# Optimization experiments

Hardware: AMD Instinct MI355X
Metric: run time of the kernel (lower is better)

The kernel has to match this reference:

```python
import jax, jax.numpy as jnp
import numpy as np

BETA = 0.25  # commitment loss weight


def setup_inputs() -> dict:
    key = jax.random.key(0)
    k1, k2 = jax.random.split(key)
    N, K, d = 131072, 1024, 64
    z_e = jax.random.normal(k1, (N, d), dtype=jnp.float32)
    scale = 1.0 / np.sqrt(d)
    codebook = jax.random.uniform(k2, (K, d), minval=-scale, maxval=scale, dtype=jnp.float32)
    return {"z_e": z_e, "codebook": codebook}


def reference(z_e, codebook):
    d = codebook.shape[-1]
    flat = z_e.reshape(-1, d)                                  # (N, d)
    z_sq = jnp.sum(flat ** 2, axis=-1, keepdims=True)          # (N, 1)
    c_sq = jnp.sum(codebook ** 2, axis=-1)[None, :]            # (1, K)
    zc = flat @ codebook.T                                     # (N, K)
    dists = z_sq - 2.0 * zc + c_sq
    idx_flat = jnp.argmin(dists, axis=-1)                      # (N,)
    e_flat = codebook[idx_flat]                                # (N, d)
    z_q_flat_st = flat + jax.lax.stop_gradient(e_flat - flat)  # straight-through
    codebook_loss = jnp.mean((e_flat - jax.lax.stop_gradient(flat)) ** 2)
    commitment_loss = jnp.mean((jax.lax.stop_gradient(e_flat) - flat) ** 2)
    vq_loss = codebook_loss + BETA * commitment_loss
    indices = idx_flat.reshape(z_e.shape[:-1])
    z_q_st = z_q_flat_st.reshape(z_e.shape)
    return (indices, z_q_st, vq_loss)
```

## Files before the change

kernel.cpp:

```cpp
#include <hip/hip_runtime.h>
#include <stdint.h>

#define DIM 64
#define KC 1024
#define HALF 512
#define ROWS_PER_BLOCK 512
#define TAU 5.0e-4f
typedef float f32x4 __attribute__((ext_vector_type(4)));
typedef short short8 __attribute__((ext_vector_type(8)));

__device__ __forceinline__ unsigned short bf16_rn(float f) {
  union { float f; uint32_t u; } v; v.f = f;
  uint32_t u = v.u;
  uint32_t r = u + 0x7fffu + ((u >> 16) & 1u);
  return (unsigned short)(r >> 16);
}
__device__ __forceinline__ float bf16_f32(unsigned short h) {
  union { uint32_t u; float f; } v; v.u = ((uint32_t)h) << 16;
  return v.f;
}
__device__ __forceinline__ void gll16(const void* g, void* l) {
  __builtin_amdgcn_global_load_lds(
      (const __attribute__((address_space(1))) void*)g,
      (__attribute__((address_space(3))) void*)l, 16, 0, 0);
}

__global__ void k1_prep(const float* __restrict__ cb,
                        unsigned short* __restrict__ cb_hi,
                        unsigned short* __restrict__ cb_lo,
                        float* __restrict__ csqh) {
  const int k = blockIdx.x, j = threadIdx.x;
  const float c = cb[k * DIM + j];
  const unsigned short hi = bf16_rn(c);
  const float hif = bf16_f32(hi);
  cb_hi[k * DIM + j] = hi;
  cb_lo[k * DIM + j] = bf16_rn(c - hif);
  float s = c * c;
  #pragma unroll
  for (int off = 32; off >= 1; off >>= 1) s += __shfl_xor(s, off);
  if (j == 0) csqh[k] = -0.5f * s;
}

__launch_bounds__(1024, 4)
__global__ void k2_argmin(const float* __restrict__ z,
                          const unsigned short* __restrict__ cb_hi,
                          const unsigned short* __restrict__ cb_lo,
                          const float* __restrict__ csqh,
                          const float* __restrict__ cb,
                          float* __restrict__ out_idx,
                          float* __restrict__ zq,
                          unsigned char* __restrict__ fl,
                          float* __restrict__ partials) {
  __shared__ unsigned short lds_cb[2 * HALF * DIM];
  __shared__ float lds_csq[KC];
  __shared__ float wpart[16];

  const int tid  = threadIdx.x;
  const int lane = tid & 63;
  const int wv   = tid >> 6;
  const int lg   = lane >> 4;
  const int lr   = lane & 15;
  const int row0 = blockIdx.x * ROWS_PER_BLOCK;

#define STAGE(h)                                                              \
  {                                                                           \
    _Pragma("unroll")                                                         \
    for (int p = 0; p < 8; ++p) {                                             \
      const int linear = p * 1024 + tid;                                      \
      const int ch = linear & 7;                                              \
      const int cl = (linear >> 3) & (HALF - 1);                              \
      const int split = linear >> 12;                                         \
      const unsigned short* src =                                             \
          (split ? cb_lo : cb_hi) + ((h) * HALF + cl) * DIM + ((ch ^ (cl & 7)) * 8); \
      gll16(src, (char*)lds_cb + linear * 16);                                \
    }                                                                         \
  }

  STAGE(0);
  if (tid < KC / 4) ((f32x4*)lds_csq)[tid] = ((const f32x4*)csqh)[tid];

  short8 zhi[2][2], zlo[2][2];
  float zsq[2];
  #pragma unroll
  for (int rt = 0; rt < 2; ++rt) {
    const int row = row0 + wv * 32 + rt * 16 + lr;
    float sq = 0.0f;
    #pragma unroll
    for (int ks = 0; ks < 2; ++ks) {
      const float* p = z + (size_t)row * DIM + ks * 32 + lg * 8;
      const f32x4 va = *(const f32x4*)p;
      const f32x4 vb = *(const f32x4*)(p + 4);
      sq = fmaf(va[0], va[0], sq); sq = fmaf(va[1], va[1], sq);
      sq = fmaf(va[2], va[2], sq); sq = fmaf(va[3], va[3], sq);
      sq = fmaf(vb[0], vb[0], sq); sq = fmaf(vb[1], vb[1], sq);
      sq = fmaf(vb[2], vb[2], sq); sq = fmaf(vb[3], vb[3], sq);
      union { uint32_t w[4]; short8 s8; } H, L;
      #pragma unroll
      for (int pr = 0; pr < 4; ++pr) {
        const float f0 = (pr < 2) ? va[2 * pr]     : vb[2 * pr - 4];
        const float f1 = (pr < 2) ? va[2 * pr + 1] : vb[2 * pr - 3];
        const uint32_t u0 = __float_as_uint(f0);
        const uint32_t u1 = __float_as_uint(f1);
        H.w[pr] = __builtin_amdgcn_perm(u1, u0, 0x07060302u);
        const float l0 = f0 - __uint_as_float(u0 & 0xffff0000u);
        const float l1 = f1 - __uint_as_float(u1 & 0xffff0000u);
        uint32_t lw;
        asm("v_cvt_pk_bf16_f32 %0, %1, %2" : "=v"(lw) : "v"(l0), "v"(l1));
        L.w[pr] = lw;
      }
      zhi[rt][ks] = H.s8;
      zlo[rt][ks] = L.s8;
    }
    zsq[rt] = sq;
  }

  float M1[2] = {-3.0e38f, -3.0e38f}, M2[2] = {-3.0e38f, -3.0e38f};
  int I1[2] = {0, 0};

  const int offh0 = lr * 128 + ((lg)     ^ (lr & 7)) * 16;
  const int offh1 = lr * 128 + ((4 + lg) ^ (lr & 7)) * 16;
  const int offl0 = offh0 + HALF * 128;
  const int offl1 = offh1 + HALF * 128;

  #pragma unroll
  for (int h = 0; h < 2; ++h) {
    __syncthreads();
    #pragma unroll 2
    for (int ct = 0; ct < HALF / 16; ++ct) {
      const int cbase = h * HALF + ct * 16 + lg * 4;
      const f32x4 init = *(const f32x4*)&lds_csq[cbase];
      const char* base = (const char*)lds_cb + ct * 2048;
      const short8 ch0 = *(const short8*)(base + offh0);
      const short8 ch1 = *(const short8*)(base + offh1);
      const short8 cl0 = *(const short8*)(base + offl0);
      const short8 cl1 = *(const short8*)(base + offl1);
      #pragma unroll
      for (int rt = 0; rt < 2; ++rt) {
        f32x4 acc = init;
        acc = __builtin_amdgcn_mfma_f32_16x16x32_bf16(ch0, zhi[rt][0], acc, 0, 0, 0);
        acc = __builtin_amdgcn_mfma_f32_16x16x32_bf16(ch1, zhi[rt][1], acc, 0, 0, 0);
        acc = __builtin_amdgcn_mfma_f32_16x16x32_bf16(ch0, zlo[rt][0], acc, 0, 0, 0);
        acc = __builtin_amdgcn_mfma_f32_16x16x32_bf16(ch1, zlo[rt][1], acc, 0, 0, 0);
        acc = __builtin_amdgcn_mfma_f32_16x16x32_bf16(cl0, zhi[rt][0], acc, 0, 0, 0);
        acc = __builtin_amdgcn_mfma_f32_16x16x32_bf16(cl1, zhi[rt][1], acc, 0, 0, 0);
        #pragma unroll
        for (int j = 0; j < 4; ++j) {
          const float s = acc[j];
          M2[rt] = __builtin_amdgcn_fmed3f(s, M1[rt], M2[rt]);
          const bool take = s > M1[rt];
          M1[rt] = fmaxf(s, M1[rt]);
          I1[rt] = take ? (cbase + j) : I1[rt];
        }
      }
    }
    __syncthreads();
    if (h == 0) STAGE(1);
  }
#undef STAGE

  float M1b[2], M2b[2], loss01 = 0.0f;
  int idxr[2];
  #pragma unroll
  for (int rt = 0; rt < 2; ++rt) {
    float m1 = M1[rt], m2 = M2[rt];
    int i1 = I1[rt];
    #pragma unroll
    for (int off = 16; off <= 32; off <<= 1) {
      const float o1 = __shfl_xor(m1, off);
      const float o2 = __shfl_xor(m2, off);
      const int   oi = __shfl_xor(i1, off);
      m2 = fmaxf(fmaxf(m2, o2), fminf(m1, o1));
      const bool take = (o1 > m1) || (o1 == m1 && oi < i1);
      if (take) { m1 = o1; i1 = oi; }
    }
    float zs = zsq[rt];
    zs += __shfl_xor(zs, 16);
    zs += __shfl_xor(zs, 32);
    M1b[rt] = m1; M2b[rt] = m2; idxr[rt] = i1;
    loss01 += zs - 2.0f * m1;
  }

  int* idxL = (int*)lds_csq;
  if (lane < 16) {
    #pragma unroll
    for (int rt = 0; rt < 2; ++rt) {
      const int r = wv * 32 + rt * 16 + lr;
      out_idx[row0 + r] = (float)idxr[rt];
      idxL[r] = idxr[rt];
      fl[row0 + r] = (M1b[rt] - M2b[rt] < TAU) ? 1 : 0;
    }
  }
  float lsum = loss01;
  #pragma unroll
  for (int off = 1; off <= 32; off <<= 1) lsum += __shfl_xor(lsum, off);
  if (lane == 0) wpart[wv] = lsum * 0.25f;
  __syncthreads();
  if (tid == 0) {
    float s = 0.0f;
    #pragma unroll
    for (int i = 0; i < 16; ++i) s += wpart[i];
    partials[blockIdx.x] = s;
  }
  {
    const int r2 = tid >> 1, halfq = tid & 1;
    const int idx = idxL[r2];
    const f32x4* src = (const f32x4*)(cb + (size_t)idx * DIM + halfq * 32);
    f32x4* dst = (f32x4*)(zq + (size_t)(row0 + r2) * DIM + halfq * 32);
    #pragma unroll
    for (int j = 0; j < 8; ++j) dst[j] = src[j];
  }
}

__global__ void k3_rescue(const float* __restrict__ z,
                          const float* __restrict__ cb,
                          const float* __restrict__ csqh,
                          const unsigned char* __restrict__ fl,
                          float* __restrict__ out_idx,
                          float* __restrict__ zq,
                          int nstripes) {
  const int lane = threadIdx.x & 63;
  const int w = blockIdx.x * 4 + (threadIdx.x >> 6);
  const int nw = gridDim.x * 4;
  for (int s = w; s < nstripes; s += nw) {
    const int base = s * 64;
    unsigned long long mask = __ballot(fl[base + lane] != 0);
    while (mask) {
      const int bit = __ffsll(mask) - 1;
      mask &= mask - 1;
      const int row = base + bit;
      const f32x4* zr4 = (const f32x4*)(z + (size_t)row * DIM);
      float m1 = -3.0e38f;
      int i1 = 0;
      for (int kk = 0; kk < 16; ++kk) {
        const int k = lane * 16 + kk;
        const f32x4* cp = (const f32x4*)(cb + (size_t)k * DIM);
        float acc = csqh[k];
        #pragma unroll
        for (int j4 = 0; j4 < DIM / 4; ++j4) {
          const f32x4 c4 = cp[j4];
          const f32x4 z4 = zr4[j4];
          acc = fmaf(z4[0], c4[0], acc);
          acc = fmaf(z4[1], c4[1], acc);
          acc = fmaf(z4[2], c4[2], acc);
          acc = fmaf(z4[3], c4[3], acc);
        }
        if (acc > m1) { m1 = acc; i1 = k; }
      }
      #pragma unroll
      for (int off = 32; off >= 1; off >>= 1) {
        const float o1 = __shfl_xor(m1, off);
        const int   oi = __shfl_xor(i1, off);
        if (o1 > m1 || (o1 == m1 && oi < i1)) { m1 = o1; i1 = oi; }
      }
      if (lane == 0) out_idx[row] = (float)i1;
      if (lane < 16)
        ((f32x4*)(zq + (size_t)row * DIM))[lane] =
            ((const f32x4*)(cb + (size_t)i1 * DIM))[lane];
    }
  }
}

__global__ void k5_reduce(const float* __restrict__ partials,
                          float* __restrict__ loss_slot,
                          float scale, int nb) {
  __shared__ float wsum[4];
  const int tid = threadIdx.x;
  float s = 0.0f;
  for (int i = tid; i < nb / 4; i += 256) {
    const f32x4 v = ((const f32x4*)partials)[i];
    s += (v[0] + v[1]) + (v[2] + v[3]);
  }
  #pragma unroll
  for (int off = 32; off >= 1; off >>= 1) s += __shfl_xor(s, off);
  if ((tid & 63) == 0) wsum[tid >> 6] = s;
  __syncthreads();
  if (tid == 0) *loss_slot = (wsum[0] + wsum[1] + wsum[2] + wsum[3]) * scale;
}

extern "C" void kernel_launch(void* const* d_in, const int* in_sizes, int n_in,
                              void* d_out, int out_size, void* d_ws, size_t ws_size,
                              hipStream_t stream) {
  const float* z  = (const float*)d_in[0];
  const float* cb = (const float*)d_in[1];
  const int N = in_sizes[0] / DIM;

  float* out       = (float*)d_out;
  float* out_idx   = out;
  float* zq        = out + N;
  float* loss_slot = out + N + (size_t)N * DIM;

  unsigned short* cb_hi = (unsigned short*)d_ws;
  unsigned short* cb_lo = cb_hi + KC * DIM;
  float* csqh = (float*)(cb_lo + KC * DIM);
  float* partials = csqh + KC;
  unsigned char* fl = (unsigned char*)(partials + 256);

  const int nb2 = N / ROWS_PER_BLOCK;
  const float scale = 1.25f / ((float)N * (float)DIM);

  k1_prep<<<KC, DIM, 0, stream>>>(cb, cb_hi, cb_lo, csqh);
  k2_argmin<<<nb2, 1024, 0, stream>>>(z, cb_hi, cb_lo, csqh, cb, out_idx, zq, fl, partials);
  k3_rescue<<<256, 256, 0, stream>>>(z, cb, csqh, fl, out_idx, zq, N / 64);
  k5_reduce<<<1, 256, 0, stream>>>(partials, loss_slot, scale, nb2);
}
```

Before: 201.9 us.

## Track best 4-column group in MFMA loop, refine with fp32 exact epilogue

The argmin inner loop now reduces each 4-wide accumulator to a single max and tracks only the winning column group, not a per-element index. An fp32 epilogue recomputes the exact scores for the 4 candidates in that group, picks the winner and sets a tighter rescue threshold. The block size drops to 512 threads and 256 rows, with the codebook staged in four quarters. The separate loss-reduce kernel is folded into the rescue kernel to save a launch. The epilogue adds some global loads and more barriers. The second-best score is now tracked per group, so near ties with an entry from the same group are only caught when those 4 candidates are recomputed.

```diff
diff --git a/kernel.cpp b/kernel.cpp
--- a/kernel.cpp
+++ b/kernel.cpp
@@ -3,9 +3,11 @@
 
 #define DIM 64
 #define KC 1024
-#define HALF 512
-#define ROWS_PER_BLOCK 512
-#define TAU 5.0e-4f
+#define QTR 256
+#define NPASS (KC / QTR)
+#define RPB 256
+#define TAU 5.0e-5f
+
 typedef float f32x4 __attribute__((ext_vector_type(4)));
 typedef short short8 __attribute__((ext_vector_type(8)));
 
@@ -32,16 +34,15 @@
   const int k = blockIdx.x, j = threadIdx.x;
   const float c = cb[k * DIM + j];
   const unsigned short hi = bf16_rn(c);
-  const float hif = bf16_f32(hi);
   cb_hi[k * DIM + j] = hi;
-  cb_lo[k * DIM + j] = bf16_rn(c - hif);
+  cb_lo[k * DIM + j] = bf16_rn(c - bf16_f32(hi));
   float s = c * c;
   #pragma unroll
   for (int off = 32; off >= 1; off >>= 1) s += __shfl_xor(s, off);
   if (j == 0) csqh[k] = -0.5f * s;
 }
 
-__launch_bounds__(1024, 4)
+__launch_bounds__(512, 4)
 __global__ void k2_argmin(const float* __restrict__ z,
                           const unsigned short* __restrict__ cb_hi,
                           const unsigned short* __restrict__ cb_lo,
@@ -51,27 +52,26 @@
                           float* __restrict__ zq,
                           unsigned char* __restrict__ fl,
                           float* __restrict__ partials) {
-  __shared__ unsigned short lds_cb[2 * HALF * DIM];
+  __shared__ unsigned short lds_cb[2 * QTR * DIM];
   __shared__ float lds_csq[KC];
-  __shared__ float wpart[16];
 
   const int tid  = threadIdx.x;
   const int lane = tid & 63;
   const int wv   = tid >> 6;
   const int lg   = lane >> 4;
   const int lr   = lane & 15;
-  const int row0 = blockIdx.x * ROWS_PER_BLOCK;
-
-#define STAGE(h)                                                              \
+  const int row0 = blockIdx.x * RPB;
+
+#define STAGE(pp)                                                             \
   {                                                                           \
     _Pragma("unroll")                                                         \
-    for (int p = 0; p < 8; ++p) {                                             \
-      const int linear = p * 1024 + tid;                                      \
+    for (int p2 = 0; p2 < 8; ++p2) {                                          \
+      const int linear = p2 * 512 + tid;                                      \
       const int ch = linear & 7;                                              \
-      const int cl = (linear >> 3) & (HALF - 1);                              \
-      const int split = linear >> 12;                                         \
+      const int cl = (linear >> 3) & (QTR - 1);                               \
+      const int split = linear >> 11;                                         \
       const unsigned short* src =                                             \
-          (split ? cb_lo : cb_hi) + ((h) * HALF + cl) * DIM + ((ch ^ (cl & 7)) * 8); \
+          (split ? cb_lo : cb_hi) + ((pp) * QTR + cl) * DIM + ((ch ^ (cl & 7)) * 8); \
       gll16(src, (char*)lds_cb + linear * 16);                                \
     }                                                                         \
   }
@@ -115,19 +115,18 @@
   }
 
   float M1[2] = {-3.0e38f, -3.0e38f}, M2[2] = {-3.0e38f, -3.0e38f};
-  int I1[2] = {0, 0};
+  int C1[2] = {0, 0};
 
   const int offh0 = lr * 128 + ((lg)     ^ (lr & 7)) * 16;
   const int offh1 = lr * 128 + ((4 + lg) ^ (lr & 7)) * 16;
-  const int offl0 = offh0 + HALF * 128;
-  const int offl1 = offh1 + HALF * 128;
-
-  #pragma unroll
-  for (int h = 0; h < 2; ++h) {
+  const int offl0 = offh0 + QTR * 128;
+  const int offl1 = offh1 + QTR * 128;
+
+  for (int p = 0; p < NPASS; ++p) {
     __syncthreads();
-    #pragma unroll 2
-    for (int ct = 0; ct < HALF / 16; ++ct) {
-      const int cbase = h * HALF + ct * 16 + lg * 4;
+    #pragma unroll 4
+    for (int ct = 0; ct < QTR / 16; ++ct) {
+      const int cbase = p * QTR + ct * 16 + lg * 4;
       const f32x4 init = *(const f32x4*)&lds_csq[cbase];
       const char* base = (const char*)lds_cb + ct * 2048;
       const short8 ch0 = *(const short8*)(base + offh0);
@@ -143,69 +142,101 @@
         acc = __builtin_amdgcn_mfma_f32_16x16x32_bf16(ch1, zlo[rt][1], acc, 0, 0, 0);
         acc = __builtin_amdgcn_mfma_f32_16x16x32_bf16(cl0, zhi[rt][0], acc, 0, 0, 0);
         acc = __builtin_amdgcn_mfma_f32_16x16x32_bf16(cl1, zhi[rt][1], acc, 0, 0, 0);
-        #pragma unroll
-        for (int j = 0; j < 4; ++j) {
-          const float s = acc[j];
-          M2[rt] = __builtin_amdgcn_fmed3f(s, M1[rt], M2[rt]);
-          const bool take = s > M1[rt];
-          M1[rt] = fmaxf(s, M1[rt]);
-          I1[rt] = take ? (cbase + j) : I1[rt];
-        }
+        const float qm = fmaxf(fmaxf(acc[0], acc[1]), fmaxf(acc[2], acc[3]));
+        M2[rt] = __builtin_amdgcn_fmed3f(qm, M1[rt], M2[rt]);
+        const bool take = qm > M1[rt];
+        M1[rt] = fmaxf(qm, M1[rt]);
+        C1[rt] = take ? cbase : C1[rt];
       }
     }
     __syncthreads();
-    if (h == 0) STAGE(1);
+    if (p < NPASS - 1) STAGE(p + 1);
   }
 #undef STAGE
 
-  float M1b[2], M2b[2], loss01 = 0.0f;
-  int idxr[2];
+  float m1f[2], m2f[2], zsf[2];
+  int cwf[2];
   #pragma unroll
   for (int rt = 0; rt < 2; ++rt) {
     float m1 = M1[rt], m2 = M2[rt];
-    int i1 = I1[rt];
+    int c1 = C1[rt];
     #pragma unroll
     for (int off = 16; off <= 32; off <<= 1) {
       const float o1 = __shfl_xor(m1, off);
       const float o2 = __shfl_xor(m2, off);
-      const int   oi = __shfl_xor(i1, off);
+      const int   oc = __shfl_xor(c1, off);
       m2 = fmaxf(fmaxf(m2, o2), fminf(m1, o1));
-      const bool take = (o1 > m1) || (o1 == m1 && oi < i1);
-      if (take) { m1 = o1; i1 = oi; }
+      const bool take = (o1 > m1) || (o1 == m1 && oc < c1);
+      if (take) { m1 = o1; c1 = oc; }
     }
     float zs = zsq[rt];
     zs += __shfl_xor(zs, 16);
     zs += __shfl_xor(zs, 32);
-    M1b[rt] = m1; M2b[rt] = m2; idxr[rt] = i1;
-    loss01 += zs - 2.0f * m1;
-  }
-
-  int* idxL = (int*)lds_csq;
-  if (lane < 16) {
+    m1f[rt] = m1; m2f[rt] = m2; cwf[rt] = c1; zsf[rt] = zs;
+  }
+
+  float* m2S   = (float*)lds_cb;
+  int*   cwS   = (int*)(m2S + 256);
+  float* zsS   = (float*)(cwS + 256);
+  float* lossS = zsS + 256;
+  int*   jS    = (int*)(lossS + 256);
+
+  if (lg == 0) {
     #pragma unroll
     for (int rt = 0; rt < 2; ++rt) {
       const int r = wv * 32 + rt * 16 + lr;
-      out_idx[row0 + r] = (float)idxr[rt];
-      idxL[r] = idxr[rt];
-      fl[row0 + r] = (M1b[rt] - M2b[rt] < TAU) ? 1 : 0;
-    }
-  }
-  float lsum = loss01;
-  #pragma unroll
-  for (int off = 1; off <= 32; off <<= 1) lsum += __shfl_xor(lsum, off);
-  if (lane == 0) wpart[wv] = lsum * 0.25f;
+      m2S[r] = m2f[rt];
+      cwS[r] = cwf[rt];
+      zsS[r] = zsf[rt];
+    }
+  }
   __syncthreads();
-  if (tid == 0) {
-    float s = 0.0f;
-    #pragma unroll
-    for (int i = 0; i < 16; ++i) s += wpart[i];
-    partials[blockIdx.x] = s;
-  }
+
   {
-    const int r2 = tid >> 1, halfq = tid & 1;
-    const int idx = idxL[r2];
-    const f32x4* src = (const f32x4*)(cb + (size_t)idx * DIM + halfq * 32);
-    f32x4* dst = (f32x4*)(zq + (size_t)(row0 + r2) * DIM + halfq * 32);
+    const int row = tid >> 1, pr = tid & 1;
+    const int cw = cwS[row];
+    const int c0 = cw + pr * 2, c1i = c0 + 1;
+    const f32x4* zr4 = (const f32x4*)(z + (size_t)(row0 + row) * DIM);
+    const f32x4* cb0 = (const f32x4*)(cb + (size_t)c0 * DIM);
+    const f32x4* cb1 = (const f32x4*)(cb + (size_t)c1i * DIM);
+    float s0 = lds_csq[c0], s1 = lds_csq[c1i];
+    #pragma unroll
+    for (int j4 = 0; j4 < 16; ++j4) {
+      const f32x4 zv = zr4[j4], a = cb0[j4], b = cb1[j4];
+      s0 = fmaf(zv[0], a[0], s0); s0 = fmaf(zv[1], a[1], s0);
+      s0 = fmaf(zv[2], a[2], s0); s0 = fmaf(zv[3], a[3], s0);
+      s1 = fmaf(zv[0], b[0], s1); s1 = fmaf(zv[1], b[1], s1);
+      s1 = fmaf(zv[2], b[2], s1); s1 = fmaf(zv[3], b[3], s1);
+    }
+    float h, l; int jh;
+    if (s0 >= s1) { h = s0; l = s1; jh = c0; } else { h = s1; l = s0; jh = c1i; }
+    const float oh = __shfl_xor(h, 1);
+    const float ol = __shfl_xor(l, 1);
+    const int   oj = __shfl_xor(jh, 1);
+    const bool takeo = (oh > h) || (oh == h && oj < jh);
+    const float sbest = takeo ? oh : h;
+    const int   jbest = takeo ? oj : jh;
+    const float second = fmaxf(fmaxf(fminf(h, oh), fmaxf(l, ol)), m2S[row]);
+    if (pr == 0) {
+      out_idx[row0 + row] = (float)jbest;
+      jS[row] = jbest;
+      fl[row0 + row] = (sbest - second < TAU) ? 1 : 0;
+      lossS[row] = zsS[row] - 2.0f * sbest;
+    }
+  }
+  __syncthreads();
+
+  if (tid < 64) {
+    float s = (lossS[tid] + lossS[tid + 64]) + (lossS[tid + 128] + lossS[tid + 192]);
+    #pragma unroll
+    for (int off = 32; off >= 1; off >>= 1) s += __shfl_xor(s, off);
+    if (tid == 0) partials[blockIdx.x] = s;
+  }
+  {
+    const int row = tid >> 1, pr = tid & 1;
+    const int jb = jS[row];
+    const f32x4* src = (const f32x4*)(cb + (size_t)jb * DIM + pr * 32);
+    f32x4* dst = (f32x4*)(zq + (size_t)(row0 + row) * DIM + pr * 32);
     #pragma unroll
     for (int j = 0; j < 8; ++j) dst[j] = src[j];
   }
@@ -217,12 +248,22 @@
                           const unsigned char* __restrict__ fl,
                           float* __restrict__ out_idx,
                           float* __restrict__ zq,
-                          int nstripes) {
+                          const float* __restrict__ partials,
+                          float* __restrict__ loss_slot,
+                          float scale, int nblocks, int nstripes) {
+  if (blockIdx.x == 0 && threadIdx.x < 64) {
+    const int lane = threadIdx.x;
+    float s = 0.0f;
+    for (int i = lane; i < nblocks; i += 64) s += partials[i];
+    #pragma unroll
+    for (int off = 32; off >= 1; off >>= 1) s += __shfl_xor(s, off);
+    if (lane == 0) *loss_slot = s * scale;
+  }
   const int lane = threadIdx.x & 63;
   const int w = blockIdx.x * 4 + (threadIdx.x >> 6);
   const int nw = gridDim.x * 4;
-  for (int s = w; s < nstripes; s += nw) {
-    const int base = s * 64;
+  for (int st = w; st < nstripes; st += nw) {
+    const int base = st * 64;
     unsigned long long mask = __ballot(fl[base + lane] != 0);
     while (mask) {
       const int bit = __ffsll(mask) - 1;
@@ -260,23 +301,6 @@
   }
 }
 
-__global__ void k5_reduce(const float* __restrict__ partials,
-                          float* __restrict__ loss_slot,
-                          float scale, int nb) {
-  __shared__ float wsum[4];
-  const int tid = threadIdx.x;
-  float s = 0.0f;
-  for (int i = tid; i < nb / 4; i += 256) {
-    const f32x4 v = ((const f32x4*)partials)[i];
-    s += (v[0] + v[1]) + (v[2] + v[3]);
-  }
-  #pragma unroll
-  for (int off = 32; off >= 1; off >>= 1) s += __shfl_xor(s, off);
-  if ((tid & 63) == 0) wsum[tid >> 6] = s;
-  __syncthreads();
-  if (tid == 0) *loss_slot = (wsum[0] + wsum[1] + wsum[2] + wsum[3]) * scale;
-}
-
 extern "C" void kernel_launch(void* const* d_in, const int* in_sizes, int n_in,
                               void* d_out, int out_size, void* d_ws, size_t ws_size,
                               hipStream_t stream) {
@@ -293,13 +317,13 @@
   unsigned short* cb_lo = cb_hi + KC * DIM;
   float* csqh = (float*)(cb_lo + KC * DIM);
   float* partials = csqh + KC;
-  unsigned char* fl = (unsigned char*)(partials + 256);
-
-  const int nb2 = N / ROWS_PER_BLOCK;
+  unsigned char* fl = (unsigned char*)(partials + 512);
+
+  const int nb2 = N / RPB;
   const float scale = 1.25f / ((float)N * (float)DIM);
 
   k1_prep<<<KC, DIM, 0, stream>>>(cb, cb_hi, cb_lo, csqh);
-  k2_argmin<<<nb2, 1024, 0, stream>>>(z, cb_hi, cb_lo, csqh, cb, out_idx, zq, fl, partials);
-  k3_rescue<<<256, 256, 0, stream>>>(z, cb, csqh, fl, out_idx, zq, N / 64);
-  k5_reduce<<<1, 256, 0, stream>>>(partials, loss_slot, scale, nb2);
-}
+  k2_argmin<<<nb2, 512, 0, stream>>>(z, cb_hi, cb_lo, csqh, cb, out_idx, zq, fl, partials);
+  k3_rescue<<<256, 256, 0, stream>>>(z, cb, csqh, fl, out_idx, zq, partials, loss_slot,
+                                     scale, nb2, N / 64);
+}
```

Result: faster. 185.7 us (-8.0%).
